# Kernel optimization log

Hardware: AMD Instinct MI355X
Metric: run time of the kernel (lower is better)

Reference implementation:

```python
import jax, jax.numpy as jnp
import numpy as np
import math

MODEL_DIM = 1024
HEAD_DIM = 64
NUM_HEADS = 16
FF_MULT = 4
FF_DIM = FF_MULT * MODEL_DIM
ATTN_DIM = NUM_HEADS * HEAD_DIM
FUSED_DIMS = (ATTN_DIM, ATTN_DIM, ATTN_DIM, FF_DIM, FF_DIM)


def setup_inputs() -> dict:
    key = jax.random.key(0)
    k_x, k_in, k_attn, k_ff = jax.random.split(key, 4)
    B, S = 2, 2048
    inputs = jax.random.normal(k_x, (B, S, MODEL_DIM), dtype=jnp.float32)
    # LayerNorm affine params (torch defaults: weight=1, bias=0)
    ln_w = jnp.ones((MODEL_DIM,), dtype=jnp.float32)
    ln_b = jnp.zeros((MODEL_DIM,), dtype=jnp.float32)
    # Linear weights stored as [in, out] (equivalent to torch W.T)
    s_in = 1.0 / math.sqrt(MODEL_DIM)
    w_in = jax.random.uniform(k_in, (MODEL_DIM, sum(FUSED_DIMS)), jnp.float32, -s_in, s_in)
    s_a = 1.0 / math.sqrt(ATTN_DIM)
    w_attn = jax.random.uniform(k_attn, (ATTN_DIM, MODEL_DIM), jnp.float32, -s_a, s_a)
    s_f = 1.0 / math.sqrt(FF_DIM)
    w_ff = jax.random.uniform(k_ff, (FF_DIM, MODEL_DIM), jnp.float32, -s_f, s_f)
    return {"inputs": inputs, "ln_w": ln_w, "ln_b": ln_b,
            "w_in": w_in, "w_attn": w_attn, "w_ff": w_ff}


def _layer_norm(x, w, b, eps=1e-5):
    mu = jnp.mean(x, axis=-1, keepdims=True)
    var = jnp.var(x, axis=-1, keepdims=True)
    return (x - mu) * jax.lax.rsqrt(var + eps) * w + b


def reference(inputs, ln_w, ln_b, w_in, w_attn, w_ff):
    B, S, D = inputs.shape
    units = _layer_norm(inputs, ln_w, ln_b)
    proj = units @ w_in                                   # [B,S,3*A+2*F]
    splits = np.cumsum(FUSED_DIMS)[:-1]
    q, k, v, ff, ff_gate = jnp.split(proj, splits, axis=-1)
    # split heads: [B,S,H*d] -> [B,H,S,d]
    def heads(t):
        return t.reshape(B, S, NUM_HEADS, HEAD_DIM).transpose(0, 2, 1, 3)
    q, k, v = heads(q), heads(k), heads(v)
    scale = 1.0 / math.sqrt(HEAD_DIM)
    score = jnp.einsum('bhsd,bhTd->bhsT', q, k) * scale   # [B,H,S,S]
    weight = jax.nn.softmax(score, axis=-1)
    attn = jnp.einsum('bhsT,bhTd->bhsd', weight, v)       # [B,H,S,d]
    concat = attn.transpose(0, 2, 1, 3).reshape(B, S, ATTN_DIM)
    attn_out = concat @ w_attn                            # [B,S,D]
    ff_out = (ff * jax.nn.gelu(ff_gate, approximate=True)) @ w_ff
    return inputs + attn_out + ff_out
```

## Files before the change

### kernel.cpp

```cpp
#include <hip/hip_runtime.h>
#include <hip/hip_bf16.h>
#include <cstdint>
#include <cstddef>

typedef __bf16 bf16;
typedef __bf16 bf16x8 __attribute__((ext_vector_type(8)));
typedef float f32x4 __attribute__((ext_vector_type(4)));

#define MFMA16(a, b, c) __builtin_amdgcn_mfma_f32_16x16x32_bf16(a, b, c, 0, 0, 0)

#define GLOBAL_LOAD_LDS16(gptr, lptr)                                          \
  __builtin_amdgcn_global_load_lds(                                            \
      (const __attribute__((address_space(1))) void*)(gptr),                   \
      (__attribute__((address_space(3))) void*)(lptr), 16, 0, 0)

__global__ __launch_bounds__(256) void prep(const float* __restrict__ w_in,
                                            const float* __restrict__ w_attn,
                                            const float* __restrict__ w_ff,
                                            bf16* __restrict__ wt_in,
                                            bf16* __restrict__ wtcat,
                                            const float* __restrict__ x,
                                            const float* __restrict__ ln_w,
                                            const float* __restrict__ ln_b,
                                            bf16* __restrict__ xn) {
  __shared__ __align__(16) char sm[4352];
  if (blockIdx.x < 16384) {
    float(*t)[33] = (float(*)[33])sm;
    int id = blockIdx.x;
    const float* src; bf16* dst;
    int srcN, srccol0, LDO, mode, obase, goff, kcol0, ntn;
    if (id < 3072) {
      src = w_in; dst = wt_in; srcN = 11264; srccol0 = 0; LDO = 1024;
      mode = 0; obase = 0; goff = 0; kcol0 = 0; ntn = 96;
    } else if (id < 7168) {
      id -= 3072; src = w_in; dst = wt_in; srcN = 11264; srccol0 = 3072;
      LDO = 1024; mode = 1; obase = 3072; goff = 0; kcol0 = 0; ntn = 128;
    } else if (id < 11264) {
      id -= 7168; src = w_in; dst = wt_in; srcN = 11264; srccol0 = 7168;
      LDO = 1024; mode = 1; obase = 3072; goff = 64; kcol0 = 0; ntn = 128;
    } else if (id < 12288) {
      id -= 11264; src = w_attn; dst = wtcat; srcN = 1024; srccol0 = 0;
      LDO = 5120; mode = 0; obase = 0; goff = 0; kcol0 = 0; ntn = 32;
    } else {
      id -= 12288; src = w_ff; dst = wtcat; srcN = 1024; srccol0 = 0;
      LDO = 5120; mode = 0; obase = 0; goff = 0; kcol0 = 1024; ntn = 32;
    }
    const int n0 = (id % ntn) * 32, k0 = (id / ntn) * 32;
    const int tx = threadIdx.x & 31, ty = threadIdx.x >> 5;
    for (int i = ty; i < 32; i += 8)
      t[i][tx] = src[(size_t)(k0 + i) * srcN + srccol0 + n0 + tx];
    __syncthreads();
    for (int i = ty; i < 32; i += 8) {
      int n = n0 + i;
      int orow = mode ? (obase + ((n >> 6) << 7) + goff + (n & 63)) : (obase + n);
      dst[(size_t)orow * LDO + kcol0 + k0 + tx] = (bf16)t[tx][i];
    }
  } else {
    float* rs = (float*)sm;
    float* rss = rs + 256;
    const int row = blockIdx.x - 16384;
    const int tid = threadIdx.x;
    const float* xr = x + (size_t)row * 1024;
    float4 v = *(const float4*)&xr[tid * 4];
    float s = v.x + v.y + v.z + v.w;
    float ss = v.x * v.x + v.y * v.y + v.z * v.z + v.w * v.w;
    rs[tid] = s; rss[tid] = ss;
    __syncthreads();
    for (int off = 128; off > 0; off >>= 1) {
      if (tid < off) { rs[tid] += rs[tid + off]; rss[tid] += rss[tid + off]; }
      __syncthreads();
    }
    const float mean = rs[0] * (1.f / 1024.f);
    const float var = rss[0] * (1.f / 1024.f) - mean * mean;
    const float rstd = rsqrtf(var + 1e-5f);
    const float* vp = (const float*)&v;
    for (int i = 0; i < 4; i++) {
      int c = tid * 4 + i;
      xn[(size_t)row * 1024 + c] = (bf16)((vp[i] - mean) * rstd * ln_w[c] + ln_b[c]);
    }
  }
}

__global__ __launch_bounds__(256) void flash_attn(const bf16* __restrict__ proj,
                                                  const bf16* __restrict__ vt,
                                                  bf16* __restrict__ hcat) {
  __shared__ __align__(16) char smem[50176];
  bf16* Ks = (bf16*)smem;
  bf16* Vs = (bf16*)(smem + 16384);
  bf16* Ps = (bf16*)(smem + 32768);
  const int tid = threadIdx.x;
  const int wave = tid >> 6, lane = tid & 63;
  const int quad = lane >> 4, l16 = lane & 15;
  const int q0 = blockIdx.x * 64;
  const int h = blockIdx.y, b = blockIdx.z;
  constexpr size_t LDP = 3072;
  const bf16* Qb = proj + (size_t)b * 2048 * LDP + h * 64;
  const bf16* Kb = proj + (size_t)b * 2048 * LDP + 1024 + h * 64;
  const bf16* Vt = vt + (size_t)(b * 16 + h) * 64 * 2048;

  const int qrow = q0 + wave * 16 + l16;
  bf16x8 aq0r = *(const bf16x8*)&Qb[(size_t)qrow * LDP + quad * 8];
  bf16x8 aq1r = *(const bf16x8*)&Qb[(size_t)qrow * LDP + 32 + quad * 8];
  bf16x8 aq0, aq1;
#pragma unroll
  for (int i = 0; i < 8; i++) {
    aq0[i] = (bf16)((float)aq0r[i] * 0.125f);
    aq1[i] = (bf16)((float)aq1r[i] * 0.125f);
  }

  f32x4 O[4] = {};
  float plrow[4] = {0.f, 0.f, 0.f, 0.f};

  const int krow_ = wave * 8 + (lane >> 3);
  const int kq_ = ((lane & 7) ^ (krow_ & 7)) * 8;
  const int vrow_ = wave * 4 + (lane >> 4);
  const int vq_ = ((lane & 15) ^ (vrow_ & 15)) * 8;

  for (int j0 = 0; j0 < 2048; j0 += 128) {
#pragma unroll
    for (int p = 0; p < 4; p++) {
      int kr = p * 32 + krow_;
      GLOBAL_LOAD_LDS16(&Kb[(size_t)(j0 + kr) * LDP + kq_],
                        &Ks[kr * 64 + (lane & 7) * 8]);
      int vr = p * 16 + vrow_;
      GLOBAL_LOAD_LDS16(&Vt[(size_t)vr * 2048 + j0 + vq_],
                        &Vs[vr * 128 + (lane & 15) * 8]);
    }
    __syncthreads();

    f32x4 sa[8];
#pragma unroll
    for (int nt = 0; nt < 8; nt++) {
      int r = nt * 16 + l16;
      bf16x8 bk0 = *(const bf16x8*)&Ks[r * 64 + (quad ^ (r & 7)) * 8];
      bf16x8 bk1 = *(const bf16x8*)&Ks[r * 64 + ((quad + 4) ^ (r & 7)) * 8];
      f32x4 t = {};
      t = MFMA16(aq0, bk0, t);
      sa[nt] = MFMA16(aq1, bk1, t);
    }

    bf16* Pw = Ps + wave * (16 * 136);
#pragma unroll
    for (int r = 0; r < 4; r++) {
      bf16* pr = &Pw[(quad * 4 + r) * 136];
      float ts = 0.f;
#pragma unroll
      for (int nt = 0; nt < 8; nt++) {
        float p = __expf(sa[nt][r]);
        pr[nt * 16 + l16] = (bf16)p;
        ts += p;
      }
      plrow[r] += ts;
    }

#pragma unroll
    for (int kg = 0; kg < 4; kg++) {
      bf16x8 aP = *(const bf16x8*)&Pw[l16 * 136 + kg * 32 + quad * 8];
#pragma unroll
      for (int nb = 0; nb < 4; nb++) {
        int vrr = nb * 16 + l16;
        int vsl = ((kg * 4 + quad) ^ (vrr & 15)) * 8;
        bf16x8 bv = *(const bf16x8*)&Vs[vrr * 128 + vsl];
        O[nb] = MFMA16(aP, bv, O[nb]);
      }
    }
    __syncthreads();
  }

#pragma unroll
  for (int r = 0; r < 4; r++) {
    float ts = plrow[r];
#pragma unroll
    for (int d = 1; d < 16; d <<= 1) ts += __shfl_xor(ts, d, 64);
    float inv = 1.f / ts;
    size_t row = (size_t)b * 2048 + q0 + wave * 16 + quad * 4 + r;
#pragma unroll
    for (int nb = 0; nb < 4; nb++)
      hcat[row * 5120 + h * 64 + nb * 16 + l16] = (bf16)(O[nb][r] * inv);
  }
}

__global__ __launch_bounds__(512, 2) void gemm_proj(const bf16* __restrict__ A,
                                                    const bf16* __restrict__ Bt,
                                                    bf16* __restrict__ proj,
                                                    bf16* __restrict__ hcat,
                                                    bf16* __restrict__ vt) {
  constexpr int K = 1024, NT = 32;
  __shared__ __align__(16) char smem[98304];
  const int tid = threadIdx.x;
  const int wave = tid >> 6, lane = tid & 63;
  const int quad = lane >> 4, l16 = lane & 15;
  const int wm0 = (wave >> 2) * 128, wn0 = (wave & 3) * 64;
  const size_t rowA0 = (size_t)blockIdx.y * 256;
  const size_t rowB0 = (size_t)blockIdx.x * 256;
  const bf16* Ag = A + rowA0 * K;
  const bf16* Bg = Bt + rowB0 * K;

  const int srow = tid >> 2;
  const int sslot = tid & 3;
  const int rslot = (quad ^ ((l16 >> 1) & 3)) * 8;

  f32x4 acc[8][4] = {};

  auto STAGE = [&](int kt, int buf) {
    bf16* As = (bf16*)(smem + buf * 32768);
    bf16* Bs = As + 256 * 32;
    const int k0 = kt * 32;
#pragma unroll
    for (int p = 0; p < 2; p++) {
      int r = p * 128 + srow;
      int kq = (sslot ^ ((r >> 1) & 3)) * 8;
      GLOBAL_LOAD_LDS16(&Ag[(size_t)r * K + k0 + kq], &As[r * 32 + sslot * 8]);
      GLOBAL_LOAD_LDS16(&Bg[(size_t)r * K + k0 + kq], &Bs[r * 32 + sslot * 8]);
    }
  };

  STAGE(0, 0);
  STAGE(1, 1);
  asm volatile("s_waitcnt vmcnt(4)" ::: "memory");
  __builtin_amdgcn_s_barrier();
  asm volatile("" ::: "memory");

  int cbuf = 0, sbuf = 2;
#pragma unroll 1
  for (int kt = 0; kt < NT; kt++) {
    if (kt + 2 < NT) STAGE(kt + 2, sbuf);
    const bf16* As = (const bf16*)(smem + cbuf * 32768);
    const bf16* Bs = As + 256 * 32;
    bf16x8 bfr[4];
#pragma unroll
    for (int j = 0; j < 4; j++)
      bfr[j] = *(const bf16x8*)&Bs[(wn0 + j * 16 + l16) * 32 + rslot];
#pragma unroll
    for (int ih = 0; ih < 2; ih++) {
      bf16x8 af[4];
#pragma unroll
      for (int i = 0; i < 4; i++)
        af[i] = *(const bf16x8*)&As[(wm0 + (ih * 4 + i) * 16 + l16) * 32 + rslot];
      __builtin_amdgcn_s_setprio(1);
#pragma unroll
      for (int i = 0; i < 4; i++)
#pragma unroll
        for (int j = 0; j < 4; j++)
          acc[ih * 4 + i][j] = MFMA16(af[i], bfr[j], acc[ih * 4 + i][j]);
      __builtin_amdgcn_s_setprio(0);
    }
    if (kt + 2 < NT) {
      asm volatile("s_waitcnt vmcnt(4)" ::: "memory");
    } else {
      asm volatile("s_waitcnt vmcnt(0)" ::: "memory");
    }
    __builtin_amdgcn_s_barrier();
    asm volatile("" ::: "memory");
    cbuf = (cbuf == 2) ? 0 : cbuf + 1;
    sbuf = (sbuf == 2) ? 0 : sbuf + 1;
  }

  {
    const int xb = (int)blockIdx.x;
    const int T2 = xb - 12;
    bf16* Cs = (bf16*)smem;
    constexpr int LDC2 = 264;
#pragma unroll 1
    for (int h = 0; h < 2; h++) {
      if ((wave >> 2) == h) {
#pragma unroll
        for (int i = 0; i < 8; i++)
#pragma unroll
          for (int j = 0; j < 4; j++)
#pragma unroll
            for (int r = 0; r < 4; r++)
              Cs[(i * 16 + quad * 4 + r) * LDC2 + wn0 + j * 16 + l16] =
                  (bf16)acc[i][j][r];
      }
      __syncthreads();
      if (xb < 8) {
#pragma unroll
        for (int it = 0; it < 8; it++) {
          int idx = it * 512 + tid;
          int row = idx >> 5, ch = (idx & 31) * 8;
          *(bf16x8*)&proj[(rowA0 + h * 128 + row) * 3072 + rowB0 + ch] =
              *(const bf16x8*)&Cs[row * LDC2 + ch];
        }
      } else if (T2 < 0) {
        const int g0 = (int)rowA0 + h * 128;
        const int bb = g0 >> 11, sloc0 = g0 & 2047;
        const int hb = (xb - 8) * 4;
        bf16* vtb = vt + ((size_t)(bb * 16 + hb) * 64) * 2048 + sloc0;
#pragma unroll
        for (int it = 0; it < 8; it++) {
          int u = it * 512 + tid;
          int col = u & 255, sc = u >> 8;
          bf16x8 o;
#pragma unroll
          for (int k = 0; k < 8; k++) o[k] = Cs[(sc * 8 + k) * LDC2 + col];
          *(bf16x8*)&vtb[(size_t)col * 2048 + sc * 8] = o;
        }
      } else {
#pragma unroll
        for (int it = 0; it < 4; it++) {
          int idx = it * 512 + tid;
          int row = idx >> 4;
          int p = (idx >> 3) & 1, c8 = (idx & 7) * 8;
          bf16x8 f = *(const bf16x8*)&Cs[row * LDC2 + p * 128 + c8];
          bf16x8 g = *(const bf16x8*)&Cs[row * LDC2 + p * 128 + 64 + c8];
          bf16x8 o;
#pragma unroll
          for (int i = 0; i < 8; i++) {
            float xg = (float)g[i];
            float u = 0.7978845608f * (xg + 0.044715f * xg * xg * xg);
            float gl = xg / (1.f + __expf(-2.f * u));
            o[i] = (bf16)((float)f[i] * gl);
          }
          *(bf16x8*)&hcat[(rowA0 + h * 128 + row) * 5120 + 1024 +
                          (2 * T2 + p) * 64 + c8] = o;
        }
      }
      __syncthreads();
    }
  }
}

__global__ __launch_bounds__(256) void gemm_out(const bf16* __restrict__ A,
                                                const bf16* __restrict__ Bt,
                                                bf16* __restrict__ part) {
  constexpr int LDAB = 5120, LDC = 136;
  __shared__ __align__(16) char smem[32768];
  bf16* As = (bf16*)smem;
  bf16* Bs = As + 128 * 64;
  bf16* Cs = (bf16*)smem;
  const int tid = threadIdx.x;
  const int wave = tid >> 6, lane = tid & 63;
  const int quad = lane >> 4, l16 = lane & 15;
  constexpr int NM = 4, NN = 4;
  const int wm0 = (wave >> 1) * 64, wn0 = (wave & 1) * 64;
  const size_t rowA0 = (size_t)blockIdx.y * 128;
  const size_t rowB0 = (size_t)blockIdx.x * 128;
  const int kbeg = blockIdx.z * 1280, kend = kbeg + 1280;

  const int srow = tid >> 3;
  const int sq = ((tid & 7) ^ (srow & 7)) * 8;
  const int sslot = (tid & 7) * 8;

  f32x4 acc[NM][NN] = {};

  for (int k0 = kbeg; k0 < kend; k0 += 64) {
#pragma unroll
    for (int p = 0; p < 4; p++) {
      int r = p * 32 + srow;
      GLOBAL_LOAD_LDS16(&A[(rowA0 + r) * LDAB + k0 + sq], &As[r * 64 + sslot]);
      GLOBAL_LOAD_LDS16(&Bt[(rowB0 + r) * LDAB + k0 + sq], &Bs[r * 64 + sslot]);
    }
    __syncthreads();
#pragma unroll
    for (int c = 0; c < 2; c++) {
      bf16x8 af[NM], bfr[NN];
#pragma unroll
      for (int i = 0; i < NM; i++) {
        int r = wm0 + i * 16 + l16;
        af[i] = *(const bf16x8*)&As[r * 64 + ((c * 4 + quad) ^ (r & 7)) * 8];
      }
#pragma unroll
      for (int j = 0; j < NN; j++) {
        int r = wn0 + j * 16 + l16;
        bfr[j] = *(const bf16x8*)&Bs[r * 64 + ((c * 4 + quad) ^ (r & 7)) * 8];
      }
#pragma unroll
      for (int i = 0; i < NM; i++)
#pragma unroll
        for (int j = 0; j < NN; j++)
          acc[i][j] = MFMA16(af[i], bfr[j], acc[i][j]);
    }
    __syncthreads();
  }

  bf16* dst = part + (size_t)blockIdx.z * (4096 * 1024);
#pragma unroll
  for (int half = 0; half < 2; half++) {
    if ((wave >> 1) == half) {
#pragma unroll
      for (int i = 0; i < NM; i++)
#pragma unroll
        for (int j = 0; j < NN; j++)
#pragma unroll
          for (int r = 0; r < 4; r++)
            Cs[(i * 16 + quad * 4 + r) * LDC + wn0 + j * 16 + l16] =
                (bf16)acc[i][j][r];
    }
    __syncthreads();
    const int c0 = (tid & 15) * 8;
#pragma unroll
    for (int it = 0; it < 4; it++) {
      int row = (tid >> 4) + it * 16;
      *(bf16x8*)&dst[(rowA0 + half * 64 + row) * 1024 + rowB0 + c0] =
          *(const bf16x8*)&Cs[row * LDC + c0];
    }
    __syncthreads();
  }
}

__global__ __launch_bounds__(256) void reduce_out(const float* __restrict__ x,
                                                  const bf16* __restrict__ part,
                                                  float* __restrict__ out) {
  const size_t i = ((size_t)blockIdx.x * 256 + threadIdx.x) * 8;
  constexpr size_t SL = 4096 * 1024;
  float r[8];
  float4 x0 = *(const float4*)&x[i];
  float4 x1 = *(const float4*)&x[i + 4];
  r[0] = x0.x; r[1] = x0.y; r[2] = x0.z; r[3] = x0.w;
  r[4] = x1.x; r[5] = x1.y; r[6] = x1.z; r[7] = x1.w;
#pragma unroll
  for (int z = 0; z < 4; z++) {
    bf16x8 p = *(const bf16x8*)&part[z * SL + i];
#pragma unroll
    for (int k = 0; k < 8; k++) r[k] += (float)p[k];
  }
  float4 o0 = {r[0], r[1], r[2], r[3]};
  float4 o1 = {r[4], r[5], r[6], r[7]};
  *(float4*)&out[i] = o0;
  *(float4*)&out[i + 4] = o1;
}

extern "C" void kernel_launch(void* const* d_in, const int* in_sizes, int n_in,
                              void* d_out, int out_size, void* d_ws, size_t ws_size,
                              hipStream_t stream) {
  const float* x      = (const float*)d_in[0];
  const float* ln_w   = (const float*)d_in[1];
  const float* ln_b   = (const float*)d_in[2];
  const float* w_in   = (const float*)d_in[3];
  const float* w_attn = (const float*)d_in[4];
  const float* w_ff   = (const float*)d_in[5];
  float* out = (float*)d_out;
  char* ws = (char*)d_ws;

  bf16* wt_in = (bf16*)(ws);
  bf16* wtcat = (bf16*)(ws + 23068672);
  bf16* xn    = (bf16*)(ws + 33554432);
  bf16* proj  = (bf16*)(ws + 41943040);
  bf16* part  = (bf16*)(ws + 67108864);
  bf16* vt    = (bf16*)(ws + 100663296);
  bf16* hcat  = (bf16*)(ws + 134217728);

  prep<<<20480, 256, 0, stream>>>(w_in, w_attn, w_ff, wt_in, wtcat,
                                  x, ln_w, ln_b, xn);
  gemm_proj<<<dim3(44, 16), 512, 0, stream>>>(xn, wt_in, proj, hcat, vt);
  flash_attn<<<dim3(32, 16, 2), 256, 0, stream>>>(proj, vt, hcat);
  gemm_out<<<dim3(8, 32, 4), 256, 0, stream>>>(hcat, wtcat, part);
  reduce_out<<<2048, 256, 0, stream>>>(x, part, out);
}
```

Baseline: 387.3 us.

## Use 64x64 vectorized weight transpose tiles and 4-stage projection GEMM pipeline

The weight prep kernel now transposes 64x64 tiles and writes eight packed bf16 values per store, replacing scalar 32x32 tiles. This cuts the block count and the number of narrow global writes. The projection GEMM moves from a 3-buffer to a 4-buffer LDS ring that prefetches three k-tiles ahead, to hide more global latency. LDS use grows to 128KB per block, which with launch bounds of 2 blocks per CU may exceed the LDS budget and reduce occupancy to one block.

```diff
diff --git a/kernel.cpp b/kernel.cpp
--- a/kernel.cpp
+++ b/kernel.cpp
@@ -23,43 +23,49 @@
                                             const float* __restrict__ ln_w,
                                             const float* __restrict__ ln_b,
                                             bf16* __restrict__ xn) {
-  __shared__ __align__(16) char sm[4352];
-  if (blockIdx.x < 16384) {
-    float(*t)[33] = (float(*)[33])sm;
+  __shared__ __align__(16) float t[64][65];
+  const int tid = threadIdx.x;
+  if (blockIdx.x < 4096) {
     int id = blockIdx.x;
     const float* src; bf16* dst;
-    int srcN, srccol0, LDO, mode, obase, goff, kcol0, ntn;
-    if (id < 3072) {
-      src = w_in; dst = wt_in; srcN = 11264; srccol0 = 0; LDO = 1024;
-      mode = 0; obase = 0; goff = 0; kcol0 = 0; ntn = 96;
-    } else if (id < 7168) {
-      id -= 3072; src = w_in; dst = wt_in; srcN = 11264; srccol0 = 3072;
-      LDO = 1024; mode = 1; obase = 3072; goff = 0; kcol0 = 0; ntn = 128;
-    } else if (id < 11264) {
-      id -= 7168; src = w_in; dst = wt_in; srcN = 11264; srccol0 = 7168;
-      LDO = 1024; mode = 1; obase = 3072; goff = 64; kcol0 = 0; ntn = 128;
-    } else if (id < 12288) {
-      id -= 11264; src = w_attn; dst = wtcat; srcN = 1024; srccol0 = 0;
-      LDO = 5120; mode = 0; obase = 0; goff = 0; kcol0 = 0; ntn = 32;
+    int srcN, n0, k0, kcol0;
+    size_t LDO;
+    bool win;
+    if (id < 2816) {
+      src = w_in; dst = wt_in; srcN = 11264; LDO = 1024;
+      n0 = (id % 176) * 64; k0 = (id / 176) * 64; kcol0 = 0; win = true;
+    } else if (id < 3072) {
+      id -= 2816; src = w_attn; dst = wtcat; srcN = 1024; LDO = 5120;
+      n0 = (id % 16) * 64; k0 = (id / 16) * 64; kcol0 = 0; win = false;
     } else {
-      id -= 12288; src = w_ff; dst = wtcat; srcN = 1024; srccol0 = 0;
-      LDO = 5120; mode = 0; obase = 0; goff = 0; kcol0 = 1024; ntn = 32;
-    }
-    const int n0 = (id % ntn) * 32, k0 = (id / ntn) * 32;
-    const int tx = threadIdx.x & 31, ty = threadIdx.x >> 5;
-    for (int i = ty; i < 32; i += 8)
-      t[i][tx] = src[(size_t)(k0 + i) * srcN + srccol0 + n0 + tx];
-    __syncthreads();
-    for (int i = ty; i < 32; i += 8) {
-      int n = n0 + i;
-      int orow = mode ? (obase + ((n >> 6) << 7) + goff + (n & 63)) : (obase + n);
-      dst[(size_t)orow * LDO + kcol0 + k0 + tx] = (bf16)t[tx][i];
+      id -= 3072; src = w_ff; dst = wtcat; srcN = 1024; LDO = 5120;
+      n0 = (id % 16) * 64; k0 = (id / 16) * 64; kcol0 = 1024; win = false;
+    }
+    int drow0;
+    if (!win || n0 < 3072) {
+      drow0 = n0;
+    } else if (n0 < 7168) {
+      int m = n0 - 3072; drow0 = 3072 + ((m >> 6) << 7);
+    } else {
+      int m = n0 - 7168; drow0 = 3072 + ((m >> 6) << 7) + 64;
+    }
+#pragma unroll
+    for (int i = 0; i < 16; i++) {
+      int k = i * 4 + (tid >> 6), n = tid & 63;
+      t[k][n] = src[(size_t)(k0 + k) * srcN + n0 + n];
+    }
+    __syncthreads();
+#pragma unroll
+    for (int j = 0; j < 2; j++) {
+      int n = j * 32 + (tid >> 3), kc = (tid & 7) * 8;
+      bf16x8 o;
+#pragma unroll
+      for (int u = 0; u < 8; u++) o[u] = (bf16)t[kc + u][n];
+      *(bf16x8*)&dst[(size_t)(drow0 + n) * LDO + kcol0 + k0 + kc] = o;
     }
   } else {
-    float* rs = (float*)sm;
-    float* rss = rs + 256;
-    const int row = blockIdx.x - 16384;
-    const int tid = threadIdx.x;
+    __shared__ float rs[256], rss[256];
+    const int row = blockIdx.x - 4096;
     const float* xr = x + (size_t)row * 1024;
     float4 v = *(const float4*)&xr[tid * 4];
     float s = v.x + v.y + v.z + v.w;
@@ -186,7 +192,7 @@
                                                     bf16* __restrict__ hcat,
                                                     bf16* __restrict__ vt) {
   constexpr int K = 1024, NT = 32;
-  __shared__ __align__(16) char smem[98304];
+  __shared__ __align__(16) char smem[131072];
   const int tid = threadIdx.x;
   const int wave = tid >> 6, lane = tid & 63;
   const int quad = lane >> 4, l16 = lane & 15;
@@ -217,15 +223,15 @@
 
   STAGE(0, 0);
   STAGE(1, 1);
-  asm volatile("s_waitcnt vmcnt(4)" ::: "memory");
+  STAGE(2, 2);
+  asm volatile("s_waitcnt vmcnt(8)" ::: "memory");
   __builtin_amdgcn_s_barrier();
   asm volatile("" ::: "memory");
 
-  int cbuf = 0, sbuf = 2;
 #pragma unroll 1
   for (int kt = 0; kt < NT; kt++) {
-    if (kt + 2 < NT) STAGE(kt + 2, sbuf);
-    const bf16* As = (const bf16*)(smem + cbuf * 32768);
+    if (kt + 3 < NT) STAGE(kt + 3, (kt + 3) & 3);
+    const bf16* As = (const bf16*)(smem + (kt & 3) * 32768);
     const bf16* Bs = As + 256 * 32;
     bf16x8 bfr[4];
 #pragma unroll
@@ -245,15 +251,15 @@
           acc[ih * 4 + i][j] = MFMA16(af[i], bfr[j], acc[ih * 4 + i][j]);
       __builtin_amdgcn_s_setprio(0);
     }
-    if (kt + 2 < NT) {
+    if (kt < NT - 3) {
+      asm volatile("s_waitcnt vmcnt(8)" ::: "memory");
+    } else if (kt == NT - 3) {
       asm volatile("s_waitcnt vmcnt(4)" ::: "memory");
     } else {
       asm volatile("s_waitcnt vmcnt(0)" ::: "memory");
     }
     __builtin_amdgcn_s_barrier();
     asm volatile("" ::: "memory");
-    cbuf = (cbuf == 2) ? 0 : cbuf + 1;
-    sbuf = (sbuf == 2) ? 0 : sbuf + 1;
   }
 
   {
@@ -441,8 +447,8 @@
   bf16* vt    = (bf16*)(ws + 100663296);
   bf16* hcat  = (bf16*)(ws + 134217728);
 
-  prep<<<20480, 256, 0, stream>>>(w_in, w_attn, w_ff, wt_in, wtcat,
-                                  x, ln_w, ln_b, xn);
+  prep<<<8192, 256, 0, stream>>>(w_in, w_attn, w_ff, wt_in, wtcat,
+                                 x, ln_w, ln_b, xn);
   gemm_proj<<<dim3(44, 16), 512, 0, stream>>>(xn, wt_in, proj, hcat, vt);
   flash_attn<<<dim3(32, 16, 2), 256, 0, stream>>>(proj, vt, hcat);
   gemm_out<<<dim3(8, 32, 4), 256, 0, stream>>>(hcat, wtcat, part);
```

New measurement: 378.4 us. -2.3%, faster.
